# Kernel tuning notes

Hardware: AMD Instinct MI355X
Metric: run time of the kernel (lower is better)

Reference implementation:

```python
import jax, jax.numpy as jnp
import numpy as np

B, T, C, H = 2, 2048, 1024, 16

def setup_inputs() -> dict:
    key = jax.random.key(0)
    ks = jax.random.split(key, 6)
    s = 1.0 / np.sqrt(C)
    return {
        "x": jax.random.normal(ks[0], (B, T, C), jnp.float32),
        "Wq": jax.random.normal(ks[1], (C, C), jnp.float32) * s,
        "Wk": jax.random.normal(ks[2], (C, C), jnp.float32) * s,
        "Wv": jax.random.normal(ks[3], (C, C), jnp.float32) * s,
        "Wp": jax.random.normal(ks[4], (C, C), jnp.float32) * s,
        "bp": jnp.zeros((C,), jnp.float32),
    }

def reference(x, Wq, Wk, Wv, Wp, bp):
    b, t, c = x.shape
    hd = c // H  # head dim
    # Linear layers: torch nn.Linear computes x @ W.T
    def split_heads(y):
        return y.reshape(b, t, H, hd).transpose(0, 2, 1, 3)  # [B,H,T,hd]
    q = split_heads(x @ Wq.T)
    k = split_heads(x @ Wk.T)
    v = split_heads(x @ Wv.T)
    scale = hd ** -0.5
    wei = jnp.einsum('bhqd,bhkd->bhqk', q, k) * scale  # [B,H,T,T]
    causal = jnp.tril(jnp.ones((t, t), bool))
    wei = jnp.where(causal, wei, -jnp.inf)
    wei = jax.nn.softmax(wei, axis=-1)
    out = jnp.einsum('bhqk,bhkd->bhqd', wei, v)  # [B,H,T,hd]
    out = out.transpose(0, 2, 1, 3).reshape(b, t, c)
    return out @ Wp.T + bp
```

## Files before the change

kernel.cpp:

```cpp
#include <hip/hip_runtime.h>
#include <hip/hip_bf16.h>
#include <stdint.h>

#define B_ 2
#define T_ 2048
#define C_ 1024
#define H_ 16
#define HD_ 64
#define NTOK (B_*T_)

typedef __bf16 bf16;
typedef bf16 bf16x4 __attribute__((ext_vector_type(4)));
typedef bf16 bf16x8 __attribute__((ext_vector_type(8)));
typedef float f32x4 __attribute__((ext_vector_type(4)));

static __device__ __forceinline__ f32x4 mfma16(bf16x8 a, bf16x8 b, f32x4 c) {
  return __builtin_amdgcn_mfma_f32_16x16x32_bf16(a, b, c, 0, 0, 0);
}

static __device__ __forceinline__ void gload_lds16(const void* g, void* l) {
  __builtin_amdgcn_global_load_lds(
      (__attribute__((address_space(1))) void*)g,
      (__attribute__((address_space(3))) void*)l, 16, 0, 0);
}

__global__ void cvt_f32_bf16(const float* __restrict__ src, bf16* __restrict__ dst, int n4) {
  int i = blockIdx.x * blockDim.x + threadIdx.x;
  if (i >= n4) return;
  float4 v = reinterpret_cast<const float4*>(src)[i];
  bf16x4 o;
  o.x = (bf16)v.x; o.y = (bf16)v.y; o.z = (bf16)v.z; o.w = (bf16)v.w;
  reinterpret_cast<bf16x4*>(dst)[i] = o;
}

__global__ void cvt4_f32_bf16(const float* __restrict__ s0, const float* __restrict__ s1,
                              const float* __restrict__ s2, const float* __restrict__ s3,
                              bf16* __restrict__ d0, bf16* __restrict__ d1,
                              bf16* __restrict__ d2, bf16* __restrict__ d3, int n4) {
  int i = blockIdx.x * blockDim.x + threadIdx.x;
  if (i >= n4) return;
  const float* src = (blockIdx.y == 0) ? s0 : (blockIdx.y == 1) ? s1 : (blockIdx.y == 2) ? s2 : s3;
  bf16* dst = (blockIdx.y == 0) ? d0 : (blockIdx.y == 1) ? d1 : (blockIdx.y == 2) ? d2 : d3;
  float4 v = reinterpret_cast<const float4*>(src)[i];
  bf16x4 o;
  o.x = (bf16)v.x; o.y = (bf16)v.y; o.z = (bf16)v.z; o.w = (bf16)v.w;
  reinterpret_cast<bf16x4*>(dst)[i] = o;
}

__global__ __launch_bounds__(256) void qkv_gemm(
    const bf16* __restrict__ X,
    const bf16* __restrict__ Wq, const bf16* __restrict__ Wk, const bf16* __restrict__ Wv,
    bf16* __restrict__ Q, bf16* __restrict__ K, bf16* __restrict__ VT) {
  __shared__ bf16 As[128 * 32];
  __shared__ bf16 Bs[128 * 32];
  const int z = blockIdx.z;
  const bf16* W = (z == 0) ? Wq : (z == 1) ? Wk : Wv;
  const int n0 = blockIdx.x * 128;
  const int o0 = blockIdx.y * 128;
  const int tid = threadIdx.x;
  const int lane = tid & 63;
  const int w = tid >> 6;
  const int wr = w >> 1, wc = w & 1;
  const int l15 = lane & 15, lhi = lane >> 4;

  f32x4 acc[4][4] = {};

  const int ca = tid;
  const int cb = tid + 256;
  const int rowa = ca >> 2, cola = (ca & 3) * 8;
  const int rowb = cb >> 2, colb = (cb & 3) * 8;

  for (int k0 = 0; k0 < C_; k0 += 32) {
    __syncthreads();
    gload_lds16(X + (size_t)(n0 + rowa) * C_ + k0 + cola, (char*)As + ca * 16);
    gload_lds16(X + (size_t)(n0 + rowb) * C_ + k0 + colb, (char*)As + cb * 16);
    gload_lds16(W + (size_t)(o0 + rowa) * C_ + k0 + cola, (char*)Bs + ca * 16);
    gload_lds16(W + (size_t)(o0 + rowb) * C_ + k0 + colb, (char*)Bs + cb * 16);
    __syncthreads();
    bf16x8 a[4], b[4];
#pragma unroll
    for (int m = 0; m < 4; m++)
      a[m] = *reinterpret_cast<const bf16x8*>(&As[(wr * 64 + m * 16 + l15) * 32 + lhi * 8]);
#pragma unroll
    for (int n = 0; n < 4; n++)
      b[n] = *reinterpret_cast<const bf16x8*>(&Bs[(wc * 64 + n * 16 + l15) * 32 + lhi * 8]);
#pragma unroll
    for (int m = 0; m < 4; m++)
#pragma unroll
      for (int n = 0; n < 4; n++)
        acc[m][n] = mfma16(a[m], b[n], acc[m][n]);
  }

  const float QSCALE = 0.125f * 1.44269504f;
#pragma unroll
  for (int m = 0; m < 4; m++) {
#pragma unroll
    for (int n = 0; n < 4; n++) {
#pragma unroll
      for (int r = 0; r < 4; r++) {
        int tok = n0 + wr * 64 + m * 16 + lhi * 4 + r;
        int o = o0 + wc * 64 + n * 16 + l15;
        int bb = tok >> 11, t = tok & (T_ - 1);
        int h = o >> 6, d = o & 63;
        float v = acc[m][n][r];
        if (z == 0) {
          Q[((size_t)(bb * H_ + h) * T_ + t) * HD_ + d] = (bf16)(v * QSCALE);
        } else if (z == 1) {
          K[((size_t)(bb * H_ + h) * T_ + t) * HD_ + d] = (bf16)v;
        } else {
          VT[((size_t)(bb * H_ + h) * HD_ + d) * T_ + t] = (bf16)v;
        }
      }
    }
  }
}

__global__ __launch_bounds__(512) void attn_kernel(
    const bf16* __restrict__ Q, const bf16* __restrict__ K,
    const bf16* __restrict__ VT, bf16* __restrict__ att) {
  __shared__ bf16 Kt[2][64 * 64];
  __shared__ bf16 Vt[2][64 * 64];
  __shared__ bf16 P[8][16][72];
  const int tid = threadIdx.x;
  const int lane = tid & 63;
  const int w = tid >> 6;
  const int l15 = lane & 15, lhi = lane >> 4;
  const int bh = blockIdx.x;
  const int b = bh >> 4, h = bh & 15;
  const int qt = (int)gridDim.y - 1 - (int)blockIdx.y;
  const int qw0 = qt * 128 + w * 16;
  const bf16* Qb = Q + (size_t)bh * T_ * HD_;
  const bf16* Kb = K + (size_t)bh * T_ * HD_;
  const bf16* Vb = VT + (size_t)bh * HD_ * T_;

  bf16x8 q[2];
#pragma unroll
  for (int kk = 0; kk < 2; kk++)
    q[kk] = *reinterpret_cast<const bf16x8*>(&Qb[(size_t)(qw0 + l15) * HD_ + kk * 32 + lhi * 8]);

  f32x4 o_acc[4] = {};
  float l_part[4] = {0.f, 0.f, 0.f, 0.f};

  const int nt = 2 * qt + 2;

  const int c0 = tid;
  const int r0 = c0 >> 3, x0 = (c0 & 7) ^ (r0 & 7);

#define STAGE(tt, bb)                                                                \
  do {                                                                               \
    int kv = (tt) * 64;                                                              \
    gload_lds16(Kb + (size_t)(kv + r0) * HD_ + x0 * 8, (char*)&Kt[bb][0] + c0 * 16); \
    gload_lds16(Vb + (size_t)r0 * T_ + kv + x0 * 8, (char*)&Vt[bb][0] + c0 * 16);    \
  } while (0)

  STAGE(0, 0);
  __syncthreads();
  int cur = 0;

  for (int it = 0; it < nt; ++it) {
    const int kv0 = it * 64;
    if (it + 1 < nt) STAGE(it + 1, cur ^ 1);

    if (kv0 <= qw0 + 15) {
      f32x4 s[4] = {};
#pragma unroll
      for (int n = 0; n < 4; n++) {
        const int krow = n * 16 + l15;
#pragma unroll
        for (int kk = 0; kk < 2; kk++) {
          const int kx = (kk * 4 + lhi) ^ (l15 & 7);
          bf16x8 kf = *reinterpret_cast<const bf16x8*>(
              (const char*)&Kt[cur][0] + krow * 128 + kx * 16);
          s[n] = mfma16(q[kk], kf, s[n]);
        }
      }

      if (kv0 + 63 > qw0) {
#pragma unroll
        for (int n = 0; n < 4; n++) {
          int key = kv0 + n * 16 + l15;
#pragma unroll
          for (int r = 0; r < 4; r++) {
            if (key > qw0 + lhi * 4 + r) s[n][r] = -1e30f;
          }
        }
      }
#pragma unroll
      for (int n = 0; n < 4; n++) {
#pragma unroll
        for (int r = 0; r < 4; r++) {
          float p = __builtin_amdgcn_exp2f(s[n][r]);
          s[n][r] = p;
          l_part[r] += p;
        }
      }
#pragma unroll
      for (int n = 0; n < 4; n++)
#pragma unroll
        for (int r = 0; r < 4; r++)
          P[w][lhi * 4 + r][n * 16 + l15] = (bf16)s[n][r];
      bf16x8 pa[2];
#pragma unroll
      for (int kk = 0; kk < 2; kk++)
        pa[kk] = *reinterpret_cast<const bf16x8*>(&P[w][l15][kk * 32 + lhi * 8]);
#pragma unroll
      for (int n = 0; n < 4; n++) {
        const int vrow = n * 16 + l15;
#pragma unroll
        for (int kk = 0; kk < 2; kk++) {
          const int vx = (kk * 4 + lhi) ^ (l15 & 7);
          bf16x8 vf = *reinterpret_cast<const bf16x8*>(
              (const char*)&Vt[cur][0] + vrow * 128 + vx * 16);
          o_acc[n] = mfma16(pa[kk], vf, o_acc[n]);
        }
      }
    }
    __syncthreads();
    cur ^= 1;
  }
#undef STAGE

  float li[4];
#pragma unroll
  for (int r = 0; r < 4; r++) {
    float v = l_part[r];
    v += __shfl_xor(v, 1);
    v += __shfl_xor(v, 2);
    v += __shfl_xor(v, 4);
    v += __shfl_xor(v, 8);
    li[r] = 1.f / v;
  }
#pragma unroll
  for (int n = 0; n < 4; n++) {
#pragma unroll
    for (int r = 0; r < 4; r++) {
      int t = qw0 + lhi * 4 + r;
      int d = n * 16 + l15;
      att[((size_t)(b * T_ + t) * H_ + h) * HD_ + d] = (bf16)(o_acc[n][r] * li[r]);
    }
  }
}

__global__ __launch_bounds__(256) void proj_gemm(
    const bf16* __restrict__ A, const bf16* __restrict__ Wp,
    const float* __restrict__ bp, float* __restrict__ out) {
  __shared__ bf16 As[128 * 32];
  __shared__ bf16 Bs[128 * 32];
  const int n0 = blockIdx.x * 128;
  const int o0 = blockIdx.y * 128;
  const int tid = threadIdx.x;
  const int lane = tid & 63;
  const int w = tid >> 6;
  const int wr = w >> 1, wc = w & 1;
  const int l15 = lane & 15, lhi = lane >> 4;

  f32x4 acc[4][4] = {};

  const int ca = tid;
  const int cb = tid + 256;
  const int rowa = ca >> 2, cola = (ca & 3) * 8;
  const int rowb = cb >> 2, colb = (cb & 3) * 8;

  for (int k0 = 0; k0 < C_; k0 += 32) {
    __syncthreads();
    gload_lds16(A + (size_t)(n0 + rowa) * C_ + k0 + cola, (char*)As + ca * 16);
    gload_lds16(A + (size_t)(n0 + rowb) * C_ + k0 + colb, (char*)As + cb * 16);
    gload_lds16(Wp + (size_t)(o0 + rowa) * C_ + k0 + cola, (char*)Bs + ca * 16);
    gload_lds16(Wp + (size_t)(o0 + rowb) * C_ + k0 + colb, (char*)Bs + cb * 16);
    __syncthreads();
    bf16x8 a[4], b[4];
#pragma unroll
    for (int m = 0; m < 4; m++)
      a[m] = *reinterpret_cast<const bf16x8*>(&As[(wr * 64 + m * 16 + l15) * 32 + lhi * 8]);
#pragma unroll
    for (int n = 0; n < 4; n++)
      b[n] = *reinterpret_cast<const bf16x8*>(&Bs[(wc * 64 + n * 16 + l15) * 32 + lhi * 8]);
#pragma unroll
    for (int m = 0; m < 4; m++)
#pragma unroll
      for (int n = 0; n < 4; n++)
        acc[m][n] = mfma16(a[m], b[n], acc[m][n]);
  }

#pragma unroll
  for (int m = 0; m < 4; m++) {
#pragma unroll
    for (int n = 0; n < 4; n++) {
#pragma unroll
      for (int r = 0; r < 4; r++) {
        int tok = n0 + wr * 64 + m * 16 + lhi * 4 + r;
        int o = o0 + wc * 64 + n * 16 + l15;
        out[(size_t)tok * C_ + o] = acc[m][n][r] + bp[o];
      }
    }
  }
}

extern "C" void kernel_launch(void* const* d_in, const int* in_sizes, int n_in,
                              void* d_out, int out_size, void* d_ws, size_t ws_size,
                              hipStream_t stream) {
  const float* x  = (const float*)d_in[0];
  const float* Wq = (const float*)d_in[1];
  const float* Wk = (const float*)d_in[2];
  const float* Wv = (const float*)d_in[3];
  const float* Wp = (const float*)d_in[4];
  const float* bp = (const float*)d_in[5];
  float* out = (float*)d_out;

  char* ws = (char*)d_ws;
  size_t off = 0;
  bf16* xb  = (bf16*)(ws + off); off += (size_t)NTOK * C_ * 2;
  bf16* wqb = (bf16*)(ws + off); off += (size_t)C_ * C_ * 2;
  bf16* wkb = (bf16*)(ws + off); off += (size_t)C_ * C_ * 2;
  bf16* wvb = (bf16*)(ws + off); off += (size_t)C_ * C_ * 2;
  bf16* wpb = (bf16*)(ws + off); off += (size_t)C_ * C_ * 2;
  bf16* Qd  = (bf16*)(ws + off); off += (size_t)NTOK * C_ * 2;
  bf16* Kd  = (bf16*)(ws + off); off += (size_t)NTOK * C_ * 2;
  bf16* VTd = (bf16*)(ws + off); off += (size_t)NTOK * C_ * 2;
  bf16* att = (bf16*)(ws + off); off += (size_t)NTOK * C_ * 2;
  (void)ws_size; (void)out_size; (void)in_sizes; (void)n_in;

  int n4 = NTOK * C_ / 4;
  cvt_f32_bf16<<<(n4 + 255) / 256, 256, 0, stream>>>(x, xb, n4);
  n4 = C_ * C_ / 4;
  cvt4_f32_bf16<<<dim3((n4 + 255) / 256, 4), 256, 0, stream>>>(
      Wq, Wk, Wv, Wp, wqb, wkb, wvb, wpb, n4);

  qkv_gemm<<<dim3(NTOK / 128, C_ / 128, 3), 256, 0, stream>>>(xb, wqb, wkb, wvb, Qd, Kd, VTd);
  attn_kernel<<<dim3(B_ * H_, T_ / 128), 512, 0, stream>>>(Qd, Kd, VTd, att);
  proj_gemm<<<dim3(NTOK / 128, C_ / 128), 256, 0, stream>>>(att, wpb, bp, out);
}
```

Before: 114.1 us.

## Give each attention wave two query tiles and store P transposed with packed converts

The attention block drops from 8 waves of 16 query rows to 4 waves of 32 rows. Each wave reuses every K and V fragment read from LDS for two MFMAs, and K/V staging is spread over fewer threads. The S MFMA operands are swapped so each lane holds one query row's scores across keys. This lets P be written to LDS as packed bf16 pairs via v_cvt_pk_bf16 and row sums be reduced with fewer shuffles. The aim is to cut LDS traffic and conversion work, at the cost of higher register pressure and fewer waves per block.

```diff
diff --git a/kernel.cpp b/kernel.cpp
--- a/kernel.cpp
+++ b/kernel.cpp
@@ -22,6 +22,12 @@
   __builtin_amdgcn_global_load_lds(
       (__attribute__((address_space(1))) void*)g,
       (__attribute__((address_space(3))) void*)l, 16, 0, 0);
+}
+
+static __device__ __forceinline__ uint32_t cvt_pk_bf16(float lo, float hi) {
+  uint32_t r;
+  asm("v_cvt_pk_bf16_f32 %0, %1, %2" : "=v"(r) : "v"(lo), "v"(hi));
+  return r;
 }
 
 __global__ void cvt_f32_bf16(const float* __restrict__ src, bf16* __restrict__ dst, int n4) {
@@ -115,12 +121,12 @@
   }
 }
 
-__global__ __launch_bounds__(512) void attn_kernel(
+__global__ __launch_bounds__(256, 3) void attn_kernel(
     const bf16* __restrict__ Q, const bf16* __restrict__ K,
     const bf16* __restrict__ VT, bf16* __restrict__ att) {
   __shared__ bf16 Kt[2][64 * 64];
   __shared__ bf16 Vt[2][64 * 64];
-  __shared__ bf16 P[8][16][72];
+  __shared__ bf16 P[4][32][72];
   const int tid = threadIdx.x;
   const int lane = tid & 63;
   const int w = tid >> 6;
@@ -128,29 +134,35 @@
   const int bh = blockIdx.x;
   const int b = bh >> 4, h = bh & 15;
   const int qt = (int)gridDim.y - 1 - (int)blockIdx.y;
-  const int qw0 = qt * 128 + w * 16;
+  const int qw0 = qt * 128 + w * 32;
   const bf16* Qb = Q + (size_t)bh * T_ * HD_;
   const bf16* Kb = K + (size_t)bh * T_ * HD_;
   const bf16* Vb = VT + (size_t)bh * HD_ * T_;
 
-  bf16x8 q[2];
-#pragma unroll
-  for (int kk = 0; kk < 2; kk++)
-    q[kk] = *reinterpret_cast<const bf16x8*>(&Qb[(size_t)(qw0 + l15) * HD_ + kk * 32 + lhi * 8]);
-
-  f32x4 o_acc[4] = {};
-  float l_part[4] = {0.f, 0.f, 0.f, 0.f};
+  bf16x8 q[2][2];
+#pragma unroll
+  for (int m = 0; m < 2; m++)
+#pragma unroll
+    for (int kk = 0; kk < 2; kk++)
+      q[m][kk] = *reinterpret_cast<const bf16x8*>(
+          &Qb[(size_t)(qw0 + m * 16 + l15) * HD_ + kk * 32 + lhi * 8]);
+
+  f32x4 o_acc[2][4] = {};
+  float lsum[2] = {0.f, 0.f};
 
   const int nt = 2 * qt + 2;
 
-  const int c0 = tid;
+  const int c0 = tid, c1 = tid + 256;
   const int r0 = c0 >> 3, x0 = (c0 & 7) ^ (r0 & 7);
+  const int r1 = c1 >> 3, x1 = (c1 & 7) ^ (r1 & 7);
 
 #define STAGE(tt, bb)                                                                \
   do {                                                                               \
     int kv = (tt) * 64;                                                              \
     gload_lds16(Kb + (size_t)(kv + r0) * HD_ + x0 * 8, (char*)&Kt[bb][0] + c0 * 16); \
+    gload_lds16(Kb + (size_t)(kv + r1) * HD_ + x1 * 8, (char*)&Kt[bb][0] + c1 * 16); \
     gload_lds16(Vb + (size_t)r0 * T_ + kv + x0 * 8, (char*)&Vt[bb][0] + c0 * 16);    \
+    gload_lds16(Vb + (size_t)r1 * T_ + kv + x1 * 8, (char*)&Vt[bb][0] + c1 * 16);    \
   } while (0)
 
   STAGE(0, 0);
@@ -161,8 +173,8 @@
     const int kv0 = it * 64;
     if (it + 1 < nt) STAGE(it + 1, cur ^ 1);
 
-    if (kv0 <= qw0 + 15) {
-      f32x4 s[4] = {};
+    if (kv0 <= qw0 + 31) {
+      f32x4 s[2][4] = {};
 #pragma unroll
       for (int n = 0; n < 4; n++) {
         const int krow = n * 16 + l15;
@@ -171,38 +183,47 @@
           const int kx = (kk * 4 + lhi) ^ (l15 & 7);
           bf16x8 kf = *reinterpret_cast<const bf16x8*>(
               (const char*)&Kt[cur][0] + krow * 128 + kx * 16);
-          s[n] = mfma16(q[kk], kf, s[n]);
+          s[0][n] = mfma16(kf, q[0][kk], s[0][n]);
+          s[1][n] = mfma16(kf, q[1][kk], s[1][n]);
         }
       }
 
       if (kv0 + 63 > qw0) {
 #pragma unroll
+        for (int m = 0; m < 2; m++) {
+          const int qrow = qw0 + m * 16 + l15;
+#pragma unroll
+          for (int n = 0; n < 4; n++) {
+            const int key = kv0 + n * 16 + lhi * 4;
+#pragma unroll
+            for (int r = 0; r < 4; r++) {
+              if (key + r > qrow) s[m][n][r] = -1e30f;
+            }
+          }
+        }
+      }
+#pragma unroll
+      for (int m = 0; m < 2; m++) {
+        char* pw = (char*)&P[w][m * 16 + l15][0];
+#pragma unroll
         for (int n = 0; n < 4; n++) {
-          int key = kv0 + n * 16 + l15;
-#pragma unroll
-          for (int r = 0; r < 4; r++) {
-            if (key > qw0 + lhi * 4 + r) s[n][r] = -1e30f;
-          }
-        }
-      }
-#pragma unroll
-      for (int n = 0; n < 4; n++) {
-#pragma unroll
-        for (int r = 0; r < 4; r++) {
-          float p = __builtin_amdgcn_exp2f(s[n][r]);
-          s[n][r] = p;
-          l_part[r] += p;
-        }
-      }
-#pragma unroll
-      for (int n = 0; n < 4; n++)
-#pragma unroll
-        for (int r = 0; r < 4; r++)
-          P[w][lhi * 4 + r][n * 16 + l15] = (bf16)s[n][r];
-      bf16x8 pa[2];
-#pragma unroll
-      for (int kk = 0; kk < 2; kk++)
-        pa[kk] = *reinterpret_cast<const bf16x8*>(&P[w][l15][kk * 32 + lhi * 8]);
+          float p0 = __builtin_amdgcn_exp2f(s[m][n][0]);
+          float p1 = __builtin_amdgcn_exp2f(s[m][n][1]);
+          float p2 = __builtin_amdgcn_exp2f(s[m][n][2]);
+          float p3 = __builtin_amdgcn_exp2f(s[m][n][3]);
+          lsum[m] += (p0 + p1) + (p2 + p3);
+          uint32_t lo = cvt_pk_bf16(p0, p1);
+          uint32_t hi = cvt_pk_bf16(p2, p3);
+          *reinterpret_cast<uint2*>(pw + (4 * n + lhi) * 8) = make_uint2(lo, hi);
+        }
+      }
+      bf16x8 pa[2][2];
+#pragma unroll
+      for (int m = 0; m < 2; m++)
+#pragma unroll
+        for (int kk = 0; kk < 2; kk++)
+          pa[m][kk] = *reinterpret_cast<const bf16x8*>(
+              (const char*)&P[w][m * 16 + l15][0] + kk * 64 + lhi * 16);
 #pragma unroll
       for (int n = 0; n < 4; n++) {
         const int vrow = n * 16 + l15;
@@ -211,7 +232,8 @@
           const int vx = (kk * 4 + lhi) ^ (l15 & 7);
           bf16x8 vf = *reinterpret_cast<const bf16x8*>(
               (const char*)&Vt[cur][0] + vrow * 128 + vx * 16);
-          o_acc[n] = mfma16(pa[kk], vf, o_acc[n]);
+          o_acc[0][n] = mfma16(pa[0][kk], vf, o_acc[0][n]);
+          o_acc[1][n] = mfma16(pa[1][kk], vf, o_acc[1][n]);
         }
       }
     }
@@ -220,23 +242,26 @@
   }
 #undef STAGE
 
-  float li[4];
-#pragma unroll
-  for (int r = 0; r < 4; r++) {
-    float v = l_part[r];
-    v += __shfl_xor(v, 1);
-    v += __shfl_xor(v, 2);
-    v += __shfl_xor(v, 4);
-    v += __shfl_xor(v, 8);
-    li[r] = 1.f / v;
-  }
-#pragma unroll
-  for (int n = 0; n < 4; n++) {
+  float lred[2];
+#pragma unroll
+  for (int m = 0; m < 2; m++) {
+    float v = lsum[m];
+    v += __shfl_xor(v, 16);
+    v += __shfl_xor(v, 32);
+    lred[m] = v;
+  }
+#pragma unroll
+  for (int m = 0; m < 2; m++) {
 #pragma unroll
     for (int r = 0; r < 4; r++) {
-      int t = qw0 + lhi * 4 + r;
-      int d = n * 16 + l15;
-      att[((size_t)(b * T_ + t) * H_ + h) * HD_ + d] = (bf16)(o_acc[n][r] * li[r]);
+      float rs = __shfl(lred[m], (lane & 48) + lhi * 4 + r);
+      float li = 1.f / rs;
+      int t = qw0 + m * 16 + lhi * 4 + r;
+#pragma unroll
+      for (int n = 0; n < 4; n++) {
+        int d = n * 16 + l15;
+        att[((size_t)(b * T_ + t) * H_ + h) * HD_ + d] = (bf16)(o_acc[m][n][r] * li);
+      }
     }
   }
 }
@@ -327,6 +352,6 @@
       Wq, Wk, Wv, Wp, wqb, wkb, wvb, wpb, n4);
 
   qkv_gemm<<<dim3(NTOK / 128, C_ / 128, 3), 256, 0, stream>>>(xb, wqb, wkb, wvb, Qd, Kd, VTd);
-  attn_kernel<<<dim3(B_ * H_, T_ / 128), 512, 0, stream>>>(Qd, Kd, VTd, att);
+  attn_kernel<<<dim3(B_ * H_, T_ / 128), 256, 0, stream>>>(Qd, Kd, VTd, att);
   proj_gemm<<<dim3(NTOK / 128, C_ / 128), 256, 0, stream>>>(att, wpb, bp, out);
 }
```

Measured after the change: 115.9 us. Within noise of the previous version (+1.6%).
